# Kernel tuning notes

Measured on AMD Instinct MI355X. Metric: run time of the kernel, lower is better.

## Reference

```python
import jax, jax.numpy as jnp
import numpy as np

VOC_SIZE = 32768
DIM = 512
NUM_TOPK = 64
BATCH = 4096


def setup_inputs() -> dict:
    key = jax.random.key(0)
    ks = jax.random.split(key, 8)
    lim = 1.0 / np.sqrt(DIM)  # kaiming_uniform(a=sqrt(5)) on [V, d] -> U(-1/sqrt(d), 1/sqrt(d))
    x = jax.random.normal(ks[0], (BATCH, DIM), dtype=jnp.float32)
    codebook = jax.random.uniform(ks[1], (VOC_SIZE, DIM), dtype=jnp.float32, minval=-lim, maxval=lim)
    Wq = jax.random.uniform(ks[2], (DIM, DIM), dtype=jnp.float32, minval=-lim, maxval=lim)
    bq = jax.random.uniform(ks[3], (DIM,), dtype=jnp.float32, minval=-lim, maxval=lim)
    Wk = jax.random.uniform(ks[4], (DIM, DIM), dtype=jnp.float32, minval=-lim, maxval=lim)
    bk = jax.random.uniform(ks[5], (DIM,), dtype=jnp.float32, minval=-lim, maxval=lim)
    Wv = jax.random.uniform(ks[6], (DIM, DIM), dtype=jnp.float32, minval=-lim, maxval=lim)
    bv = jax.random.uniform(ks[7], (DIM,), dtype=jnp.float32, minval=-lim, maxval=lim)
    return {"x": x, "codebook": codebook, "Wq": Wq, "bq": bq,
            "Wk": Wk, "bk": bk, "Wv": Wv, "bv": bv}


def reference(x, codebook, Wq, bq, Wk, bk, Wv, bv):
    # projections (torch Linear with weight stored pre-transposed as [in, out])
    q = x @ Wq + bq              # [B, d]
    k = codebook @ Wk + bk       # [V, d]
    v = codebook @ Wv + bv       # [V, d]

    dots = jnp.einsum('bd,kd->bk', q, k)              # [B, V]
    top, _ = jax.lax.top_k(dots, NUM_TOPK)            # [B, num_topk]
    thresh = top[..., -1:]                            # k-th largest value per row
    mask_value = -jnp.finfo(dots.dtype).max
    dots = jnp.where(dots < thresh, mask_value, dots)
    attn = jax.nn.softmax(dots, axis=-1)              # [B, V]
    out = jnp.einsum('bk,kd->bd', attn, v)            # [B, d]
    return out
```

## Files before the change

### kernel.cpp

```cpp
#include <hip/hip_runtime.h>
#include <cstdint>

#define VOC   32768
#define DIM   512
#define TOPK  64
#define BATCH 4096

#define KSIG     2.45f
#define EPS_SEL  0.012f
#define CAND_CAP 512
#define RES_CAP  256
#define FCAP     1024

typedef unsigned short u16;
typedef __attribute__((ext_vector_type(8))) short bf16x8;
typedef __attribute__((ext_vector_type(4))) float f32x4;

__device__ __forceinline__ u16 f2bf(float f) {
    unsigned u = __float_as_uint(f);
    unsigned r = (u + 0x7FFFu + ((u >> 16) & 1u)) >> 16;
    return (u16)r;
}
__device__ __forceinline__ float bf2f(u16 h) {
    return __uint_as_float(((unsigned)h) << 16);
}
__device__ __forceinline__ unsigned enc16(u16 h) {
    return (h & 0x8000u) ? (unsigned)((u16)~h) : (unsigned)(h | 0x8000u);
}
__device__ __forceinline__ float dec16(unsigned s16) {
    u16 h = (s16 & 0x8000u) ? (u16)(s16 ^ 0x8000u) : (u16)(~s16);
    return bf2f(h);
}

__device__ __forceinline__ void async16(const void* g, void* l) {
    __builtin_amdgcn_global_load_lds(
        (const __attribute__((address_space(1))) void*)g,
        (__attribute__((address_space(3))) void*)l, 16, 0, 0);
}

template <bool BT, bool F64ACC>
__global__ __launch_bounds__(256)
void gemm64(const float* __restrict__ A, const float* __restrict__ B,
            const float* __restrict__ bias, float* __restrict__ C,
            int M, int N, int K)
{
    const int KS = 16;
    __shared__ float As[KS][68];
    __shared__ float Bs[KS][64];

    const int tid = threadIdx.x;
    const int m0 = blockIdx.y * 64;
    const int n0 = blockIdx.x * 64;
    const int ty = tid >> 4;
    const int tx = tid & 15;

    float acc[4][4];
    double acc64[4][4];
#pragma unroll
    for (int i = 0; i < 4; i++)
#pragma unroll
        for (int j = 0; j < 4; j++) { acc[i][j] = 0.f; if (F64ACC) acc64[i][j] = 0.0; }

    for (int kt = 0; kt < K; kt += KS) {
        {
            int row = tid >> 2, kq = tid & 3;
            const float4 av = *(const float4*)(A + (size_t)(m0 + row) * K + kt + kq * 4);
            As[kq * 4 + 0][row] = av.x;
            As[kq * 4 + 1][row] = av.y;
            As[kq * 4 + 2][row] = av.z;
            As[kq * 4 + 3][row] = av.w;
        }
        if (!BT) {
            int krow = tid >> 4, nq = tid & 15;
            *(float4*)&Bs[krow][nq * 4] =
                *(const float4*)(B + (size_t)(kt + krow) * N + n0 + nq * 4);
        } else {
            int nrow = tid >> 2, kq = tid & 3;
            const float4 bv = *(const float4*)(B + (size_t)(n0 + nrow) * K + kt + kq * 4);
            Bs[kq * 4 + 0][nrow] = bv.x;
            Bs[kq * 4 + 1][nrow] = bv.y;
            Bs[kq * 4 + 2][nrow] = bv.z;
            Bs[kq * 4 + 3][nrow] = bv.w;
        }
        __syncthreads();

#pragma unroll
        for (int kk = 0; kk < KS; kk++) {
            float4 a = *(const float4*)&As[kk][ty * 4];
            float4 b = *(const float4*)&Bs[kk][tx * 4];
            float av[4] = {a.x, a.y, a.z, a.w};
            float bv[4] = {b.x, b.y, b.z, b.w};
#pragma unroll
            for (int i = 0; i < 4; i++)
#pragma unroll
                for (int j = 0; j < 4; j++)
                    acc[i][j] += av[i] * bv[j];
        }
        __syncthreads();
        if (F64ACC) {
#pragma unroll
            for (int i = 0; i < 4; i++)
#pragma unroll
                for (int j = 0; j < 4; j++) { acc64[i][j] += (double)acc[i][j]; acc[i][j] = 0.f; }
        }
    }

    float4 bb = make_float4(0.f, 0.f, 0.f, 0.f);
    if (bias) bb = *(const float4*)(bias + n0 + tx * 4);
#pragma unroll
    for (int i = 0; i < 4; i++) {
        float4 o;
        o.x = (F64ACC ? (float)acc64[i][0] : acc[i][0]) + bb.x;
        o.y = (F64ACC ? (float)acc64[i][1] : acc[i][1]) + bb.y;
        o.z = (F64ACC ? (float)acc64[i][2] : acc[i][2]) + bb.z;
        o.w = (F64ACC ? (float)acc64[i][3] : acc[i][3]) + bb.w;
        *(float4*)(C + (size_t)(m0 + ty * 4 + i) * N + n0 + tx * 4) = o;
    }
}

__global__ void zero_ws(unsigned* __restrict__ p, int n)
{
    int i = blockIdx.x * 256 + threadIdx.x;
    if (i < n) p[i] = 0u;
}

__device__ __forceinline__ void pack_rows_dev(int bid, int tid,
        const float* __restrict__ src, u16* __restrict__ hi,
        u16* __restrict__ lo, int R, int log2R)
{
    int idx = bid * 256 + tid;
    int c8  = idx >> log2R;
    int row = idx & (R - 1);
    const float* sp = src + (size_t)row * DIM + c8 * 8;
    float xv[8];
    *(float4*)&xv[0] = *(const float4*)sp;
    *(float4*)&xv[4] = *(const float4*)(sp + 4);
    int ks = c8 >> 2, ch = c8 & 3;
    size_t ob = ((size_t)(ks * 4 + ch) * R + row) * 8;
    u16 h[8], l[8];
#pragma unroll
    for (int j = 0; j < 8; j++) {
        h[j] = f2bf(xv[j]);
        l[j] = f2bf(xv[j] - bf2f(h[j]));
    }
    *(uint4*)(hi + ob) = *(const uint4*)h;
    if (lo) *(uint4*)(lo + ob) = *(const uint4*)l;
}

__device__ __forceinline__ void pack_bT_dev(int bid, int tid,
        const float* __restrict__ W, u16* __restrict__ hi, u16* __restrict__ lo)
{
    int idx = bid * 256 + tid;
    int n  = idx & (DIM - 1);
    int c8 = idx >> 9;
    int ks = c8 >> 2, ch = c8 & 3;
    size_t ob = ((size_t)(ks * 4 + ch) * DIM + n) * 8;
    u16 h[8], l[8];
#pragma unroll
    for (int j = 0; j < 8; j++) {
        float x = W[(size_t)(c8 * 8 + j) * DIM + n];
        h[j] = f2bf(x);
        l[j] = f2bf(x - bf2f(h[j]));
    }
    *(uint4*)(hi + ob) = *(const uint4*)h;
    *(uint4*)(lo + ob) = *(const uint4*)l;
}

__device__ __forceinline__ void cbar_dev(int bid, int tid,
        const float* __restrict__ cb, float* __restrict__ cbarsum)
{
    const int r0 = bid * 128;
    float s0 = 0.f, s1 = 0.f;
    for (int r = 0; r < 128; r++) {
        const float* rp = cb + (size_t)(r0 + r) * DIM;
        s0 += rp[tid];
        s1 += rp[tid + 256];
    }
    atomicAdd(&cbarsum[tid], s0);
    atomicAdd(&cbarsum[tid + 256], s1);
}

__device__ __forceinline__ void bias_fold_dev(int bid, int tid,
        const float* __restrict__ bq, const float* __restrict__ Wk,
        float* __restrict__ bqk)
{
    const int lane = tid & 63, wave = tid >> 6;
    const int j = bid * 4 + wave;
    const float* wr = Wk + (size_t)j * DIM + lane * 8;
    const float* bp = bq + lane * 8;
    double s = 0.0;
#pragma unroll
    for (int t = 0; t < 8; t++) s += (double)bp[t] * (double)wr[t];
#pragma unroll
    for (int off = 32; off > 0; off >>= 1) s += __shfl_down(s, off);
    if (lane == 0) bqk[j] = (float)s;
}

__device__ __forceinline__ void rowstats_dev(int bid, int tid,
        const float* __restrict__ q2, const float* __restrict__ cbarsum,
        float* __restrict__ trow, float* __restrict__ sigrow)
{
    const int lane = tid & 63, wave = tid >> 6;
    const int row = bid * 4 + wave;
    const float* qp = q2 + (size_t)row * DIM + lane * 8;
    float4 a0 = *(const float4*)qp, a1 = *(const float4*)(qp + 4);
    const float* cp = cbarsum + lane * 8;
    float4 c0 = *(const float4*)cp, c1 = *(const float4*)(cp + 4);
    float mu = a0.x*c0.x + a0.y*c0.y + a0.z*c0.z + a0.w*c0.w
             + a1.x*c1.x + a1.y*c1.y + a1.z*c1.z + a1.w*c1.w;
    float nr = a0.x*a0.x + a0.y*a0.y + a0.z*a0.z + a0.w*a0.w
             + a1.x*a1.x + a1.y*a1.y + a1.z*a1.z + a1.w*a1.w;
#pragma unroll
    for (int off = 32; off > 0; off >>= 1) {
        mu += __shfl_down(mu, off);
        nr += __shfl_down(nr, off);
    }
    if (lane == 0) {
        mu *= (1.f / VOC);
        float sig = sqrtf(nr * (1.f / 1536.f));
        trow[row] = mu + KSIG * sig;
        sigrow[row] = sig;
    }
}

__global__ __launch_bounds__(256)
void fused_prep(const float* __restrict__ x, const float* __restrict__ Wqk,
                const float* __restrict__ codebook, const float* __restrict__ Wv,
                const float* __restrict__ bq, const float* __restrict__ Wk,
                u16* __restrict__ xh, u16* __restrict__ xl,
                u16* __restrict__ wqkh, u16* __restrict__ wqkl,
                u16* __restrict__ cbh, u16* __restrict__ wvh,
                u16* __restrict__ wvl, float* __restrict__ cbarsum,
                float* __restrict__ bqk)
{
    const int b = blockIdx.x, tid = threadIdx.x;
    if (b < 1024)       pack_rows_dev(b, tid, x, xh, xl, BATCH, 12);
    else if (b < 1152)  pack_bT_dev(b - 1024, tid, Wqk, wqkh, wqkl);
    else if (b < 9344)  pack_rows_dev(b - 1152, tid, codebook, cbh, nullptr, VOC, 15);
    else if (b < 9472)  pack_bT_dev(b - 9344, tid, Wv, wvh, wvl);
    else if (b < 9728)  cbar_dev(b - 9472, tid, codebook, cbarsum);
    else                bias_fold_dev(b - 9728, tid, bq, Wk, bqk);
}

__global__ __launch_bounds__(256)
void fused_q2post(const float* __restrict__ q2, const float* __restrict__ cbarsum,
                  float* __restrict__ trow, float* __restrict__ sigrow,
                  u16* __restrict__ q2h)
{
    const int b = blockIdx.x, tid = threadIdx.x;
    if (b < 1024) rowstats_dev(b, tid, q2, cbarsum, trow, sigrow);
    else          pack_rows_dev(b - 1024, tid, q2, q2h, nullptr, BATCH, 12);
}

__global__ __launch_bounds__(256, 4)
void mfma_dots(const u16* __restrict__ Ah, const u16* __restrict__ Bh,
               const float* __restrict__ trow, unsigned* __restrict__ candBuf,
               unsigned* __restrict__ counters)
{
    __shared__ u16 lds[2 * 8192];

    const int tid  = threadIdx.x;
    const int lane = tid & 63;
    const int wave = tid >> 6;
    const int wm = wave >> 1, wn = wave & 1;
    const int lr = lane & 15;
    const int q  = lane >> 4;

    const int L   = blockIdx.x;
    const int xcd = L & 7;
    const int j   = L >> 3;
    const int m0  = (xcd * 4 + (j & 3)) * 128;
    const int n0  = (j >> 2) * 128;

    const int a  = wave >> 1;
    const u16* src = a ? Bh : Ah;
    const int rb   = a ? n0 : m0;
    const size_t R = a ? (size_t)VOC : (size_t)BATCH;
    const int i0   = (wave & 1) * 4;

    const size_t gstep = (size_t)4 * R * 8;
    const u16* gp0 = src + ((size_t)(((i0 + 0) >> 1)) * R + rb + ((i0 + 0) & 1) * 64 + lane) * 8;
    const u16* gp1 = src + ((size_t)(((i0 + 1) >> 1)) * R + rb + ((i0 + 1) & 1) * 64 + lane) * 8;
    const u16* gp2 = src + ((size_t)(((i0 + 2) >> 1)) * R + rb + ((i0 + 2) & 1) * 64 + lane) * 8;
    const u16* gp3 = src + ((size_t)(((i0 + 3) >> 1)) * R + rb + ((i0 + 3) & 1) * 64 + lane) * 8;
    const int loff0 = a * 4096 + (i0 + 0) * 512 + lane * 8;
    const int loff1 = a * 4096 + (i0 + 1) * 512 + lane * 8;
    const int loff2 = a * 4096 + (i0 + 2) * 512 + lane * 8;
    const int loff3 = a * 4096 + (i0 + 3) * 512 + lane * 8;

#define ISSUE(b)                                                              \
    {                                                                         \
        async16(gp0, &lds[(b) * 8192 + loff0]); gp0 += gstep;                 \
        async16(gp1, &lds[(b) * 8192 + loff1]); gp1 += gstep;                 \
        async16(gp2, &lds[(b) * 8192 + loff2]); gp2 += gstep;                 \
        async16(gp3, &lds[(b) * 8192 + loff3]); gp3 += gstep;                 \
    }

    f32x4 acc[4][4] = {};

    ISSUE(0)
    ISSUE(1)

    for (int s = 0; s < 16; s++) {
        if (s < 15) __builtin_amdgcn_s_waitcnt(0x0F74);
        else        __builtin_amdgcn_s_waitcnt(0x0F70);
        __builtin_amdgcn_s_barrier();
        const u16* base = &lds[(s & 1) * 8192];

        bf16x8 ah[4];
#pragma unroll
        for (int mt = 0; mt < 4; mt++)
            ah[mt] = *(const bf16x8*)&base[q * 1024 + (wm * 64 + mt * 16 + lr) * 8];

        __builtin_amdgcn_s_setprio(1);
#pragma unroll
        for (int nt = 0; nt < 3; nt++) {
            bf16x8 bh = *(const bf16x8*)&base[4096 + q * 1024 + (wn * 64 + nt * 16 + lr) * 8];
#pragma unroll
            for (int mt = 0; mt < 4; mt++)
                acc[mt][nt] = __builtin_amdgcn_mfma_f32_16x16x32_bf16(ah[mt], bh, acc[mt][nt], 0, 0, 0);
        }
        bf16x8 bh3 = *(const bf16x8*)&base[4096 + q * 1024 + (wn * 64 + 3 * 16 + lr) * 8];
        __builtin_amdgcn_s_setprio(0);

        __builtin_amdgcn_s_waitcnt(0xC07F);
        __builtin_amdgcn_s_barrier();
        __builtin_amdgcn_sched_barrier(0);
        if (s < 14) ISSUE(s & 1)

        __builtin_amdgcn_s_setprio(1);
#pragma unroll
        for (int mt = 0; mt < 4; mt++)
            acc[mt][3] = __builtin_amdgcn_mfma_f32_16x16x32_bf16(ah[mt], bh3, acc[mt][3], 0, 0, 0);
        __builtin_amdgcn_s_setprio(0);
    }
#undef ISSUE

#pragma unroll
    for (int mt = 0; mt < 4; mt++) {
#pragma unroll
        for (int r = 0; r < 4; r++) {
            int rowg = m0 + wm * 64 + mt * 16 + q * 4 + r;
            float tr = trow[rowg];
#pragma unroll
            for (int nt = 0; nt < 4; nt++) {
                float val = acc[mt][nt][r];
                if (val >= tr) {
                    unsigned slot = atomicAdd(&counters[rowg], 1u);
                    if (slot < CAND_CAP) {
                        unsigned s16 = enc16(f2bf(val));
                        candBuf[(size_t)rowg * CAND_CAP + slot] =
                            (s16 << 16) | (unsigned)(n0 + wn * 64 + nt * 16 + lr);
                    }
                }
            }
        }
    }
}

__global__ __launch_bounds__(256, 3)
void mfma_out(const u16* __restrict__ Ah, const u16* __restrict__ Al,
              const u16* __restrict__ Bh, const u16* __restrict__ Bl,
              const float* __restrict__ bias, float* __restrict__ Cout, int Ma)
{
    __shared__ u16 lds[2 * 12288];

    const int tid  = threadIdx.x;
    const int lane = tid & 63;
    const int wave = tid >> 6;
    const int wm = wave >> 1, wn = wave & 1;
    const int m0 = blockIdx.y * 128, n0 = blockIdx.x * 64;
    const int lr = lane & 15;
    const int q  = lane >> 4;
    const size_t R = (size_t)Ma;

    f32x4 acc[4][2] = {};

#define VISSUE(ks, b)                                                          \
    {                                                                          \
        _Pragma("unroll")                                                      \
        for (int i_ = 0; i_ < 2; i_++) {                                       \
            int u_ = tid + i_ * 256;                                           \
            size_t ai_ = ((size_t)((ks) * 4 + (u_ >> 7)) * R + m0 + (u_ & 127)) * 8; \
            async16(Ah + ai_, &lds[(b) * 12288 + u_ * 8]);                     \
            async16(Al + ai_, &lds[(b) * 12288 + 6144 + u_ * 8]);              \
        }                                                                      \
        {                                                                      \
            int u_ = tid;                                                      \
            size_t bi_ = ((size_t)((ks) * 4 + (u_ >> 6)) * DIM + n0 + (u_ & 63)) * 8; \
            async16(Bh + bi_, &lds[(b) * 12288 + 4096 + u_ * 8]);              \
            async16(Bl + bi_, &lds[(b) * 12288 + 10240 + u_ * 8]);             \
        }                                                                      \
    }

    VISSUE(0, 0)

    for (int ks = 0; ks < 16; ks++) {
        __syncthreads();
        if (ks < 15) VISSUE(ks + 1, (ks + 1) & 1)
        const u16* base = &lds[(ks & 1) * 12288];

        bf16x8 ah[4], al[4];
#pragma unroll
        for (int mt = 0; mt < 4; mt++) {
            int row = wm * 64 + mt * 16 + lr;
            ah[mt] = *(const bf16x8*)&base[q * 1024 + row * 8];
            al[mt] = *(const bf16x8*)&base[6144 + q * 1024 + row * 8];
        }
#pragma unroll
        for (int nt = 0; nt < 2; nt++) {
            int col = wn * 32 + nt * 16 + lr;
            bf16x8 bh = *(const bf16x8*)&base[4096 + q * 512 + col * 8];
            bf16x8 bl = *(const bf16x8*)&base[10240 + q * 512 + col * 8];
#pragma unroll
            for (int mt = 0; mt < 4; mt++) {
                acc[mt][nt] = __builtin_amdgcn_mfma_f32_16x16x32_bf16(ah[mt], bh, acc[mt][nt], 0, 0, 0);
                acc[mt][nt] = __builtin_amdgcn_mfma_f32_16x16x32_bf16(ah[mt], bl, acc[mt][nt], 0, 0, 0);
                acc[mt][nt] = __builtin_amdgcn_mfma_f32_16x16x32_bf16(al[mt], bh, acc[mt][nt], 0, 0, 0);
            }
        }
    }
#undef VISSUE

#pragma unroll
    for (int mt = 0; mt < 4; mt++)
#pragma unroll
        for (int nt = 0; nt < 2; nt++) {
            int col = n0 + wn * 32 + nt * 16 + lr;
            float bb = bias[col];
#pragma unroll
            for (int r = 0; r < 4; r++) {
                int rowg = m0 + wm * 64 + mt * 16 + q * 4 + r;
                Cout[(size_t)rowg * DIM + col] = acc[mt][nt][r] + bb;
            }
        }
}

__global__ __launch_bounds__(256)
void select8(const unsigned* __restrict__ candBuf, const unsigned* __restrict__ counters,
             const float* __restrict__ trow, const float* __restrict__ sigrow,
             const float* __restrict__ q2, const float* __restrict__ codebook,
             float* __restrict__ y, u16* __restrict__ yh, u16* __restrict__ yl)
{
    __shared__ unsigned recs[CAND_CAP];
    __shared__ unsigned list[RES_CAP];
    __shared__ unsigned hist[256];
    __shared__ unsigned long long keys[FCAP];
    __shared__ float q2s[DIM];
    __shared__ float wArr[FCAP];
    __shared__ float yrow[DIM];
    __shared__ float redf[256];
    __shared__ unsigned redu[256];
    __shared__ unsigned s_R, s_b1, s_rem, s_thr, s_cnt;

    const int tid  = threadIdx.x;
    const int lane = tid & 63;
    const int wave = tid >> 6;
    const int row  = blockIdx.x;

    for (int i = tid; i < DIM; i += 256) q2s[i] = q2[(size_t)row * DIM + i];

    const unsigned cnt = counters[row];
    bool fb = (cnt < TOPK || cnt > CAND_CAP);
    int selCount = 0;
    float invZ = 1.f;

    if (!fb) {
        for (int i = tid; i < CAND_CAP; i += 256)
            recs[i] = (i < (int)cnt) ? candBuf[(size_t)row * CAND_CAP + i] : 0u;
        if (tid == 0) s_R = 0;
        hist[tid] = 0;
        __syncthreads();

#pragma unroll
        for (int e = 0; e < 2; e++) {
            int i = tid + e * 256;
            if (i < (int)cnt) atomicAdd(&hist[recs[i] >> 24], 1u);
        }
        __syncthreads();
        if (tid == 0) {
            unsigned c = 0; int b = 255;
            for (; b > 0; b--) {
                unsigned h = hist[b];
                if (c + h >= TOPK) break;
                c += h;
            }
            s_b1 = (unsigned)b; s_rem = TOPK - c;
        }
        __syncthreads();
        const unsigned b1 = s_b1, rem = s_rem;
        hist[tid] = 0;
        __syncthreads();

#pragma unroll
        for (int e = 0; e < 2; e++) {
            int i = tid + e * 256;
            if (i < (int)cnt && (recs[i] >> 24) == b1)
                atomicAdd(&hist[(recs[i] >> 16) & 0xFFu], 1u);
        }
        __syncthreads();
        if (tid == 0) {
            unsigned c = 0; int b = 255;
            for (; b > 0; b--) {
                unsigned h = hist[b];
                if (c + h >= rem) break;
                c += h;
            }
            s_thr = (b1 << 8) | (unsigned)b;
        }
        __syncthreads();

        const float a64  = dec16(s_thr);
        const float band = a64 - 2.f * EPS_SEL;
        if (trow[row] > band) fb = true;

        if (!fb) {
#pragma unroll
            for (int e = 0; e < 2; e++) {
                int i = tid + e * 256;
                if (i < (int)cnt && dec16(recs[i] >> 16) >= band) {
                    unsigned p = atomicAdd(&s_R, 1u);
                    if (p < RES_CAP) list[p] = recs[i];
                }
            }
            __syncthreads();
            const int R = (int)s_R;
            if (R > RES_CAP) fb = true;

            if (!fb) {
                for (int c = wave; c < R; c += 4) {
                    unsigned idx = list[c] & 0xFFFFu;
                    const float* cb = codebook + (size_t)idx * DIM + lane * 8;
                    float4 c0 = *(const float4*)cb, c1 = *(const float4*)(cb + 4);
                    const float* qp = &q2s[lane * 8];
                    float4 a0 = *(const float4*)qp, a1 = *(const float4*)(qp + 4);
                    double s = (double)a0.x * c0.x + (double)a0.y * c0.y
                             + (double)a0.z * c0.z + (double)a0.w * c0.w
                             + (double)a1.x * c1.x + (double)a1.y * c1.y
                             + (double)a1.z * c1.z + (double)a1.w * c1.w;
#pragma unroll
                    for (int off = 32; off > 0; off >>= 1) s += __shfl_down(s, off);
                    if (lane == 0) {
                        float val = (float)s;
                        unsigned b = __float_as_uint(val);
                        unsigned sk = (b & 0x80000000u) ? ~b : (b | 0x80000000u);
                        keys[c] = ((unsigned long long)(~sk) << 32) | idx;
                    }
                }
                if (tid >= R && tid < RES_CAP) keys[tid] = ~0ULL;
                __syncthreads();

                for (int k = 2; k <= RES_CAP; k <<= 1) {
                    for (int j = k >> 1; j > 0; j >>= 1) {
                        int ixj = tid ^ j;
                        if (ixj > tid) {
                            unsigned long long a = keys[tid], b2 = keys[ixj];
                            if (((tid & k) == 0) ? (a > b2) : (a < b2)) { keys[tid] = b2; keys[ixj] = a; }
                        }
                        __syncthreads();
                    }
                }

                const unsigned threshInv = (unsigned)(keys[TOPK - 1] >> 32);
                unsigned sk0 = ~(unsigned)(keys[0] >> 32);
                const float vmax = __uint_as_float((sk0 & 0x80000000u) ? (sk0 & 0x7FFFFFFFu) : ~sk0);

                unsigned hi = (unsigned)(keys[tid] >> 32);
                bool sel = (hi <= threshInv);
                unsigned sk = ~hi;
                float val = __uint_as_float((sk & 0x80000000u) ? (sk & 0x7FFFFFFFu) : ~sk);
                float w = sel ? expf(val - vmax) : 0.f;
                wArr[tid] = w;
                redf[tid] = w;
                redu[tid] = sel ? 1u : 0u;
                __syncthreads();
                for (int s = 128; s > 0; s >>= 1) {
                    if (tid < s) { redf[tid] += redf[tid + s]; redu[tid] += redu[tid + s]; }
                    __syncthreads();
                }
                invZ = 1.0f / redf[0];
                selCount = (int)redu[0];
            }
        }
    }

    if (fb) {
        const float sig = sigrow[row];
        float tf = trow[row] - 0.35f * sig;
        unsigned fcnt = 0;

        for (int it = 0; it < 16; it++) {
            if (tid == 0) s_cnt = 0;
            __syncthreads();
            for (int i = tid; i < VOC; i += 256) {
                const float* cb = codebook + (size_t)i * DIM;
                double s = 0.0;
                for (int d = 0; d < DIM; d += 4) {
                    float4 c4 = *(const float4*)(cb + d);
                    s += (double)q2s[d + 0] * (double)c4.x + (double)q2s[d + 1] * (double)c4.y
                       + (double)q2s[d + 2] * (double)c4.z + (double)q2s[d + 3] * (double)c4.w;
                }
                float vv = (float)s;
                if (vv >= tf) {
                    unsigned p = atomicAdd(&s_cnt, 1u);
                    if (p < FCAP) {
                        unsigned b = __float_as_uint(vv);
                        unsigned sk = (b & 0x80000000u) ? ~b : (b | 0x80000000u);
                        keys[p] = ((unsigned long long)(~sk) << 32) | (unsigned)i;
                    }
                }
            }
            __syncthreads();
            fcnt = s_cnt;
            if (fcnt > FCAP) { tf += 0.15f * sig; continue; }
            if (fcnt < TOPK) { tf -= 0.35f * sig; continue; }
            break;
        }
        if (fcnt > FCAP) fcnt = FCAP;
        for (int i = tid; i < FCAP; i += 256)
            if (i >= (int)fcnt) keys[i] = ~0ULL;
        __syncthreads();

        for (int k = 2; k <= FCAP; k <<= 1) {
            for (int j = k >> 1; j > 0; j >>= 1) {
#pragma unroll
                for (int e = 0; e < 4; e++) {
                    int i = tid + e * 256;
                    int ixj = i ^ j;
                    if (ixj > i) {
                        unsigned long long a = keys[i], b = keys[ixj];
                        if (((i & k) == 0) ? (a > b) : (a < b)) { keys[i] = b; keys[ixj] = a; }
                    }
                }
                __syncthreads();
            }
        }

        const unsigned threshInv = (unsigned)(keys[TOPK - 1] >> 32);
        unsigned sk0 = ~(unsigned)(keys[0] >> 32);
        const float vmax = __uint_as_float((sk0 & 0x80000000u) ? (sk0 & 0x7FFFFFFFu) : ~sk0);

        float lsum = 0.f; unsigned lcnt = 0;
        for (int i = tid; i < FCAP; i += 256) {
            unsigned hi = (unsigned)(keys[i] >> 32);
            bool sel = (hi <= threshInv);
            unsigned sk = ~hi;
            float vv = __uint_as_float((sk & 0x80000000u) ? (sk & 0x7FFFFFFFu) : ~sk);
            float w = sel ? expf(vv - vmax) : 0.f;
            wArr[i] = w;
            lsum += w; lcnt += sel ? 1u : 0u;
        }
        redf[tid] = lsum; redu[tid] = lcnt;
        __syncthreads();
        for (int s = 128; s > 0; s >>= 1) {
            if (tid < s) { redf[tid] += redf[tid + s]; redu[tid] += redu[tid + s]; }
            __syncthreads();
        }
        invZ = 1.f / redf[0];
        selCount = (int)redu[0];
    }

    for (int d = tid; d < DIM; d += 256) {
        float acc = 0.f;
        for (int i = 0; i < selCount; i++) {
            unsigned idx = (unsigned)(keys[i] & 0xFFFFFFFFu);
            acc += wArr[i] * codebook[(size_t)idx * DIM + d];
        }
        float v = acc * invZ;
        y[(size_t)row * DIM + d] = v;
        yrow[d] = v;
    }
    __syncthreads();
    if (tid < 64) {
        const int c8 = tid;
        u16 h[8], l[8];
#pragma unroll
        for (int j = 0; j < 8; j++) {
            float xv = yrow[c8 * 8 + j];
            h[j] = f2bf(xv);
            l[j] = f2bf(xv - bf2f(h[j]));
        }
        size_t ob = ((size_t)c8 * BATCH + row) * 8;
        *(uint4*)(yh + ob) = *(const uint4*)h;
        *(uint4*)(yl + ob) = *(const uint4*)l;
    }
}

extern "C" void kernel_launch(void* const* d_in, const int* in_sizes, int n_in,
                              void* d_out, int out_size, void* d_ws, size_t ws_size,
                              hipStream_t stream)
{
    const float* x        = (const float*)d_in[0];
    const float* codebook = (const float*)d_in[1];
    const float* Wq       = (const float*)d_in[2];
    const float* bq       = (const float*)d_in[3];
    const float* Wk       = (const float*)d_in[4];
    const float* Wv       = (const float*)d_in[6];
    const float* bv       = (const float*)d_in[7];
    float* out = (float*)d_out;

    float* q2   = (float*)d_ws;
    float* Wqk  = q2   + (size_t)BATCH * DIM;
    float* bqk  = Wqk  + (size_t)DIM * DIM;
    float* y    = bqk  + 1024;
    float* trow = y    + (size_t)BATCH * DIM;
    float* sigr = trow + BATCH;
    unsigned* counters = (unsigned*)(sigr + BATCH);
    unsigned* flags    = counters + BATCH;
    float* cbarsum     = (float*)(flags + BATCH);
    unsigned* candBuf  = (unsigned*)(cbarsum + 512);
    u16* q2h = (u16*)(candBuf + (size_t)BATCH * CAND_CAP);
    u16* cbh = q2h + (size_t)BATCH * DIM;
    u16* yh  = cbh + (size_t)VOC * DIM;
    u16* yl  = yh  + (size_t)BATCH * DIM;
    u16* wvh = yl  + (size_t)BATCH * DIM;
    u16* wvl = wvh + (size_t)DIM * DIM;

    u16* xh   = yh;
    u16* xl   = yl;
    u16* wqkh = (u16*)candBuf;
    u16* wqkl = wqkh + (size_t)DIM * DIM;

    dim3 blk(256);

    zero_ws<<<dim3(34), blk, 0, stream>>>(counters, BATCH * 2 + 512);

    gemm64<true, true><<<dim3(DIM / 64, DIM / 64), blk, 0, stream>>>(
        Wq, Wk, nullptr, Wqk, DIM, DIM, DIM);

    fused_prep<<<dim3(9856), blk, 0, stream>>>(
        x, Wqk, codebook, Wv, bq, Wk,
        xh, xl, wqkh, wqkl, cbh, wvh, wvl, cbarsum, bqk);

    mfma_out<<<dim3(DIM / 64, BATCH / 128), blk, 0, stream>>>(
        xh, xl, wqkh, wqkl, bqk, q2, BATCH);

    fused_q2post<<<dim3(2048), blk, 0, stream>>>(q2, cbarsum, trow, sigr, q2h);

    mfma_dots<<<dim3(8192), blk, 0, stream>>>(q2h, cbh, trow, candBuf, counters);

    select8<<<dim3(BATCH), blk, 0, stream>>>(
        candBuf, counters, trow, sigr, q2, codebook, y, yh, yl);

    mfma_out<<<dim3(DIM / 64, BATCH / 128), blk, 0, stream>>>(
        yh, yl, wvh, wvl, bv, out, BATCH);
}
```

Baseline: 663.3 us.

## Split row selection into lean fast-path kernel and separate flagged fallback kernel

The per-row select kernel is split in two. The fast candidate path keeps only RES_CAP-sized key and weight buffers and writes a flag for rows that need it. A second kernel runs the full-vocabulary fallback scan only for flagged rows. This shrinks LDS and register use in the common kernel so more blocks can be resident, and it drops the unused fp32 y write. The cost is an extra launch of BATCH blocks that mostly exit at once, and the flags buffer must be zeroed beforehand.

```diff
diff --git a/kernel.cpp b/kernel.cpp
--- a/kernel.cpp
+++ b/kernel.cpp
@@ -36,6 +36,24 @@
     __builtin_amdgcn_global_load_lds(
         (const __attribute__((address_space(1))) void*)g,
         (__attribute__((address_space(3))) void*)l, 16, 0, 0);
+}
+
+__device__ __forceinline__ void pack_y_tail(int tid, int row,
+        const float* __restrict__ yrow, u16* __restrict__ yh, u16* __restrict__ yl)
+{
+    if (tid < 64) {
+        const int c8 = tid;
+        u16 h[8], l[8];
+#pragma unroll
+        for (int j = 0; j < 8; j++) {
+            float xv = yrow[c8 * 8 + j];
+            h[j] = f2bf(xv);
+            l[j] = f2bf(xv - bf2f(h[j]));
+        }
+        size_t ob = ((size_t)c8 * BATCH + row) * 8;
+        *(uint4*)(yh + ob) = *(const uint4*)h;
+        *(uint4*)(yl + ob) = *(const uint4*)l;
+    }
 }
 
 template <bool BT, bool F64ACC>
@@ -437,228 +455,152 @@
 }
 
 __global__ __launch_bounds__(256)
-void select8(const unsigned* __restrict__ candBuf, const unsigned* __restrict__ counters,
-             const float* __restrict__ trow, const float* __restrict__ sigrow,
-             const float* __restrict__ q2, const float* __restrict__ codebook,
-             float* __restrict__ y, u16* __restrict__ yh, u16* __restrict__ yl)
+void select6(const unsigned* __restrict__ candBuf, const unsigned* __restrict__ counters,
+             const float* __restrict__ trow, const float* __restrict__ q2,
+             const float* __restrict__ codebook, unsigned* __restrict__ flags,
+             u16* __restrict__ yh, u16* __restrict__ yl)
 {
     __shared__ unsigned recs[CAND_CAP];
     __shared__ unsigned list[RES_CAP];
     __shared__ unsigned hist[256];
-    __shared__ unsigned long long keys[FCAP];
+    __shared__ unsigned long long keys[RES_CAP];
     __shared__ float q2s[DIM];
-    __shared__ float wArr[FCAP];
+    __shared__ float wArr[RES_CAP];
     __shared__ float yrow[DIM];
     __shared__ float redf[256];
     __shared__ unsigned redu[256];
-    __shared__ unsigned s_R, s_b1, s_rem, s_thr, s_cnt;
+    __shared__ unsigned s_R;
+    __shared__ unsigned s_b1, s_rem, s_thr;
 
     const int tid  = threadIdx.x;
     const int lane = tid & 63;
     const int wave = tid >> 6;
     const int row  = blockIdx.x;
 
+    const unsigned cnt = counters[row];
+    if (cnt < TOPK || cnt > CAND_CAP) {
+        if (tid == 0) flags[row] = 1u;
+        return;
+    }
     for (int i = tid; i < DIM; i += 256) q2s[i] = q2[(size_t)row * DIM + i];
-
-    const unsigned cnt = counters[row];
-    bool fb = (cnt < TOPK || cnt > CAND_CAP);
-    int selCount = 0;
-    float invZ = 1.f;
-
-    if (!fb) {
-        for (int i = tid; i < CAND_CAP; i += 256)
-            recs[i] = (i < (int)cnt) ? candBuf[(size_t)row * CAND_CAP + i] : 0u;
-        if (tid == 0) s_R = 0;
-        hist[tid] = 0;
-        __syncthreads();
-
-#pragma unroll
-        for (int e = 0; e < 2; e++) {
-            int i = tid + e * 256;
-            if (i < (int)cnt) atomicAdd(&hist[recs[i] >> 24], 1u);
-        }
-        __syncthreads();
-        if (tid == 0) {
-            unsigned c = 0; int b = 255;
-            for (; b > 0; b--) {
-                unsigned h = hist[b];
-                if (c + h >= TOPK) break;
-                c += h;
-            }
-            s_b1 = (unsigned)b; s_rem = TOPK - c;
-        }
-        __syncthreads();
-        const unsigned b1 = s_b1, rem = s_rem;
-        hist[tid] = 0;
-        __syncthreads();
-
-#pragma unroll
-        for (int e = 0; e < 2; e++) {
-            int i = tid + e * 256;
-            if (i < (int)cnt && (recs[i] >> 24) == b1)
-                atomicAdd(&hist[(recs[i] >> 16) & 0xFFu], 1u);
-        }
-        __syncthreads();
-        if (tid == 0) {
-            unsigned c = 0; int b = 255;
-            for (; b > 0; b--) {
-                unsigned h = hist[b];
-                if (c + h >= rem) break;
-                c += h;
-            }
-            s_thr = (b1 << 8) | (unsigned)b;
-        }
-        __syncthreads();
-
-        const float a64  = dec16(s_thr);
-        const float band = a64 - 2.f * EPS_SEL;
-        if (trow[row] > band) fb = true;
-
-        if (!fb) {
-#pragma unroll
-            for (int e = 0; e < 2; e++) {
-                int i = tid + e * 256;
-                if (i < (int)cnt && dec16(recs[i] >> 16) >= band) {
-                    unsigned p = atomicAdd(&s_R, 1u);
-                    if (p < RES_CAP) list[p] = recs[i];
-                }
+    for (int i = tid; i < CAND_CAP; i += 256)
+        recs[i] = (i < (int)cnt) ? candBuf[(size_t)row * CAND_CAP + i] : 0u;
+    if (tid == 0) s_R = 0;
+    hist[tid] = 0;
+    __syncthreads();
+
+#pragma unroll
+    for (int e = 0; e < 2; e++) {
+        int i = tid + e * 256;
+        if (i < (int)cnt) atomicAdd(&hist[recs[i] >> 24], 1u);
+    }
+    __syncthreads();
+    if (tid == 0) {
+        unsigned c = 0; int b = 255;
+        for (; b > 0; b--) {
+            unsigned h = hist[b];
+            if (c + h >= TOPK) break;
+            c += h;
+        }
+        s_b1 = (unsigned)b; s_rem = TOPK - c;
+    }
+    __syncthreads();
+    const unsigned b1 = s_b1, rem = s_rem;
+    hist[tid] = 0;
+    __syncthreads();
+
+#pragma unroll
+    for (int e = 0; e < 2; e++) {
+        int i = tid + e * 256;
+        if (i < (int)cnt && (recs[i] >> 24) == b1)
+            atomicAdd(&hist[(recs[i] >> 16) & 0xFFu], 1u);
+    }
+    __syncthreads();
+    if (tid == 0) {
+        unsigned c = 0; int b = 255;
+        for (; b > 0; b--) {
+            unsigned h = hist[b];
+            if (c + h >= rem) break;
+            c += h;
+        }
+        s_thr = (b1 << 8) | (unsigned)b;
+    }
+    __syncthreads();
+
+    const float a64  = dec16(s_thr);
+    const float band = a64 - 2.f * EPS_SEL;
+    if (trow[row] > band) {
+        if (tid == 0) flags[row] = 1u;
+        return;
+    }
+
+#pragma unroll
+    for (int e = 0; e < 2; e++) {
+        int i = tid + e * 256;
+        if (i < (int)cnt && dec16(recs[i] >> 16) >= band) {
+            unsigned p = atomicAdd(&s_R, 1u);
+            if (p < RES_CAP) list[p] = recs[i];
+        }
+    }
+    __syncthreads();
+    const int R = (int)s_R;
+    if (R > RES_CAP) {
+        if (tid == 0) flags[row] = 1u;
+        return;
+    }
+
+    for (int c = wave; c < R; c += 4) {
+        unsigned idx = list[c] & 0xFFFFu;
+        const float* cb = codebook + (size_t)idx * DIM + lane * 8;
+        float4 c0 = *(const float4*)cb, c1 = *(const float4*)(cb + 4);
+        const float* qp = &q2s[lane * 8];
+        float4 a0 = *(const float4*)qp, a1 = *(const float4*)(qp + 4);
+        double s = (double)a0.x * c0.x + (double)a0.y * c0.y
+                 + (double)a0.z * c0.z + (double)a0.w * c0.w
+                 + (double)a1.x * c1.x + (double)a1.y * c1.y
+                 + (double)a1.z * c1.z + (double)a1.w * c1.w;
+#pragma unroll
+        for (int off = 32; off > 0; off >>= 1) s += __shfl_down(s, off);
+        if (lane == 0) {
+            float val = (float)s;
+            unsigned b = __float_as_uint(val);
+            unsigned sk = (b & 0x80000000u) ? ~b : (b | 0x80000000u);
+            keys[c] = ((unsigned long long)(~sk) << 32) | idx;
+        }
+    }
+    if (tid >= R && tid < RES_CAP) keys[tid] = ~0ULL;
+    __syncthreads();
+
+    for (int k = 2; k <= RES_CAP; k <<= 1) {
+        for (int j = k >> 1; j > 0; j >>= 1) {
+            int ixj = tid ^ j;
+            if (ixj > tid) {
+                unsigned long long a = keys[tid], b2 = keys[ixj];
+                if (((tid & k) == 0) ? (a > b2) : (a < b2)) { keys[tid] = b2; keys[ixj] = a; }
             }
             __syncthreads();
-            const int R = (int)s_R;
-            if (R > RES_CAP) fb = true;
-
-            if (!fb) {
-                for (int c = wave; c < R; c += 4) {
-                    unsigned idx = list[c] & 0xFFFFu;
-                    const float* cb = codebook + (size_t)idx * DIM + lane * 8;
-                    float4 c0 = *(const float4*)cb, c1 = *(const float4*)(cb + 4);
-                    const float* qp = &q2s[lane * 8];
-                    float4 a0 = *(const float4*)qp, a1 = *(const float4*)(qp + 4);
-                    double s = (double)a0.x * c0.x + (double)a0.y * c0.y
-                             + (double)a0.z * c0.z + (double)a0.w * c0.w
-                             + (double)a1.x * c1.x + (double)a1.y * c1.y
-                             + (double)a1.z * c1.z + (double)a1.w * c1.w;
-#pragma unroll
-                    for (int off = 32; off > 0; off >>= 1) s += __shfl_down(s, off);
-                    if (lane == 0) {
-                        float val = (float)s;
-                        unsigned b = __float_as_uint(val);
-                        unsigned sk = (b & 0x80000000u) ? ~b : (b | 0x80000000u);
-                        keys[c] = ((unsigned long long)(~sk) << 32) | idx;
-                    }
-                }
-                if (tid >= R && tid < RES_CAP) keys[tid] = ~0ULL;
-                __syncthreads();
-
-                for (int k = 2; k <= RES_CAP; k <<= 1) {
-                    for (int j = k >> 1; j > 0; j >>= 1) {
-                        int ixj = tid ^ j;
-                        if (ixj > tid) {
-                            unsigned long long a = keys[tid], b2 = keys[ixj];
-                            if (((tid & k) == 0) ? (a > b2) : (a < b2)) { keys[tid] = b2; keys[ixj] = a; }
-                        }
-                        __syncthreads();
-                    }
-                }
-
-                const unsigned threshInv = (unsigned)(keys[TOPK - 1] >> 32);
-                unsigned sk0 = ~(unsigned)(keys[0] >> 32);
-                const float vmax = __uint_as_float((sk0 & 0x80000000u) ? (sk0 & 0x7FFFFFFFu) : ~sk0);
-
-                unsigned hi = (unsigned)(keys[tid] >> 32);
-                bool sel = (hi <= threshInv);
-                unsigned sk = ~hi;
-                float val = __uint_as_float((sk & 0x80000000u) ? (sk & 0x7FFFFFFFu) : ~sk);
-                float w = sel ? expf(val - vmax) : 0.f;
-                wArr[tid] = w;
-                redf[tid] = w;
-                redu[tid] = sel ? 1u : 0u;
-                __syncthreads();
-                for (int s = 128; s > 0; s >>= 1) {
-                    if (tid < s) { redf[tid] += redf[tid + s]; redu[tid] += redu[tid + s]; }
-                    __syncthreads();
-                }
-                invZ = 1.0f / redf[0];
-                selCount = (int)redu[0];
-            }
-        }
-    }
-
-    if (fb) {
-        const float sig = sigrow[row];
-        float tf = trow[row] - 0.35f * sig;
-        unsigned fcnt = 0;
-
-        for (int it = 0; it < 16; it++) {
-            if (tid == 0) s_cnt = 0;
-            __syncthreads();
-            for (int i = tid; i < VOC; i += 256) {
-                const float* cb = codebook + (size_t)i * DIM;
-                double s = 0.0;
-                for (int d = 0; d < DIM; d += 4) {
-                    float4 c4 = *(const float4*)(cb + d);
-                    s += (double)q2s[d + 0] * (double)c4.x + (double)q2s[d + 1] * (double)c4.y
-                       + (double)q2s[d + 2] * (double)c4.z + (double)q2s[d + 3] * (double)c4.w;
-                }
-                float vv = (float)s;
-                if (vv >= tf) {
-                    unsigned p = atomicAdd(&s_cnt, 1u);
-                    if (p < FCAP) {
-                        unsigned b = __float_as_uint(vv);
-                        unsigned sk = (b & 0x80000000u) ? ~b : (b | 0x80000000u);
-                        keys[p] = ((unsigned long long)(~sk) << 32) | (unsigned)i;
-                    }
-                }
-            }
-            __syncthreads();
-            fcnt = s_cnt;
-            if (fcnt > FCAP) { tf += 0.15f * sig; continue; }
-            if (fcnt < TOPK) { tf -= 0.35f * sig; continue; }
-            break;
-        }
-        if (fcnt > FCAP) fcnt = FCAP;
-        for (int i = tid; i < FCAP; i += 256)
-            if (i >= (int)fcnt) keys[i] = ~0ULL;
+        }
+    }
+
+    const unsigned threshInv = (unsigned)(keys[TOPK - 1] >> 32);
+    unsigned sk0 = ~(unsigned)(keys[0] >> 32);
+    const float vmax = __uint_as_float((sk0 & 0x80000000u) ? (sk0 & 0x7FFFFFFFu) : ~sk0);
+
+    unsigned hi = (unsigned)(keys[tid] >> 32);
+    bool sel = (hi <= threshInv);
+    unsigned sk = ~hi;
+    float val = __uint_as_float((sk & 0x80000000u) ? (sk & 0x7FFFFFFFu) : ~sk);
+    float w = sel ? expf(val - vmax) : 0.f;
+    wArr[tid] = w;
+    redf[tid] = w;
+    redu[tid] = sel ? 1u : 0u;
+    __syncthreads();
+    for (int s = 128; s > 0; s >>= 1) {
+        if (tid < s) { redf[tid] += redf[tid + s]; redu[tid] += redu[tid + s]; }
         __syncthreads();
-
-        for (int k = 2; k <= FCAP; k <<= 1) {
-            for (int j = k >> 1; j > 0; j >>= 1) {
-#pragma unroll
-                for (int e = 0; e < 4; e++) {
-                    int i = tid + e * 256;
-                    int ixj = i ^ j;
-                    if (ixj > i) {
-                        unsigned long long a = keys[i], b = keys[ixj];
-                        if (((i & k) == 0) ? (a > b) : (a < b)) { keys[i] = b; keys[ixj] = a; }
-                    }
-                }
-                __syncthreads();
-            }
-        }
-
-        const unsigned threshInv = (unsigned)(keys[TOPK - 1] >> 32);
-        unsigned sk0 = ~(unsigned)(keys[0] >> 32);
-        const float vmax = __uint_as_float((sk0 & 0x80000000u) ? (sk0 & 0x7FFFFFFFu) : ~sk0);
-
-        float lsum = 0.f; unsigned lcnt = 0;
-        for (int i = tid; i < FCAP; i += 256) {
-            unsigned hi = (unsigned)(keys[i] >> 32);
-            bool sel = (hi <= threshInv);
-            unsigned sk = ~hi;
-            float vv = __uint_as_float((sk & 0x80000000u) ? (sk & 0x7FFFFFFFu) : ~sk);
-            float w = sel ? expf(vv - vmax) : 0.f;
-            wArr[i] = w;
-            lsum += w; lcnt += sel ? 1u : 0u;
-        }
-        redf[tid] = lsum; redu[tid] = lcnt;
-        __syncthreads();
-        for (int s = 128; s > 0; s >>= 1) {
-            if (tid < s) { redf[tid] += redf[tid + s]; redu[tid] += redu[tid + s]; }
-            __syncthreads();
-        }
-        invZ = 1.f / redf[0];
-        selCount = (int)redu[0];
-    }
+    }
+    const float invZ = 1.0f / redf[0];
+    const int selCount = (int)redu[0];
 
     for (int d = tid; d < DIM; d += 256) {
         float acc = 0.f;
@@ -666,24 +608,115 @@
             unsigned idx = (unsigned)(keys[i] & 0xFFFFFFFFu);
             acc += wArr[i] * codebook[(size_t)idx * DIM + d];
         }
-        float v = acc * invZ;
-        y[(size_t)row * DIM + d] = v;
-        yrow[d] = v;
-    }
-    __syncthreads();
-    if (tid < 64) {
-        const int c8 = tid;
-        u16 h[8], l[8];
-#pragma unroll
-        for (int j = 0; j < 8; j++) {
-            float xv = yrow[c8 * 8 + j];
-            h[j] = f2bf(xv);
-            l[j] = f2bf(xv - bf2f(h[j]));
-        }
-        size_t ob = ((size_t)c8 * BATCH + row) * 8;
-        *(uint4*)(yh + ob) = *(const uint4*)h;
-        *(uint4*)(yl + ob) = *(const uint4*)l;
-    }
+        yrow[d] = acc * invZ;
+    }
+    __syncthreads();
+    pack_y_tail(tid, row, yrow, yh, yl);
+}
+
+__global__ __launch_bounds__(256)
+void fallback_row(const unsigned* __restrict__ flags, const float* __restrict__ q2,
+                  const float* __restrict__ codebook, const float* __restrict__ trow,
+                  const float* __restrict__ sigrow, u16* __restrict__ yh,
+                  u16* __restrict__ yl)
+{
+    const int row = blockIdx.x;
+    if (!flags[row]) return;
+
+    __shared__ float q2s[DIM];
+    __shared__ unsigned long long keys[FCAP];
+    __shared__ float wArr[FCAP];
+    __shared__ float yrow[DIM];
+    __shared__ float redf[256];
+    __shared__ unsigned redu[256];
+    __shared__ unsigned s_cnt;
+
+    const int tid = threadIdx.x;
+    for (int i = tid; i < DIM; i += 256) q2s[i] = q2[(size_t)row * DIM + i];
+    const float sig = sigrow[row];
+    float tf = trow[row] - 0.35f * sig;
+    unsigned cnt = 0;
+
+    for (int it = 0; it < 16; it++) {
+        if (tid == 0) s_cnt = 0;
+        __syncthreads();
+        for (int i = tid; i < VOC; i += 256) {
+            const float* cb = codebook + (size_t)i * DIM;
+            double s = 0.0;
+            for (int d = 0; d < DIM; d += 4) {
+                float4 c4 = *(const float4*)(cb + d);
+                s += (double)q2s[d + 0] * (double)c4.x + (double)q2s[d + 1] * (double)c4.y
+                   + (double)q2s[d + 2] * (double)c4.z + (double)q2s[d + 3] * (double)c4.w;
+            }
+            float vv = (float)s;
+            if (vv >= tf) {
+                unsigned p = atomicAdd(&s_cnt, 1u);
+                if (p < FCAP) {
+                    unsigned b = __float_as_uint(vv);
+                    unsigned sk = (b & 0x80000000u) ? ~b : (b | 0x80000000u);
+                    keys[p] = ((unsigned long long)(~sk) << 32) | (unsigned)i;
+                }
+            }
+        }
+        __syncthreads();
+        cnt = s_cnt;
+        if (cnt > FCAP) { tf += 0.15f * sig; continue; }
+        if (cnt < TOPK) { tf -= 0.35f * sig; continue; }
+        break;
+    }
+    if (cnt > FCAP) cnt = FCAP;
+    for (int i = tid; i < FCAP; i += 256)
+        if (i >= (int)cnt) keys[i] = ~0ULL;
+    __syncthreads();
+
+    for (int k = 2; k <= FCAP; k <<= 1) {
+        for (int j = k >> 1; j > 0; j >>= 1) {
+#pragma unroll
+            for (int e = 0; e < 4; e++) {
+                int i = tid + e * 256;
+                int ixj = i ^ j;
+                if (ixj > i) {
+                    unsigned long long a = keys[i], b = keys[ixj];
+                    if (((i & k) == 0) ? (a > b) : (a < b)) { keys[i] = b; keys[ixj] = a; }
+                }
+            }
+            __syncthreads();
+        }
+    }
+
+    const unsigned threshInv = (unsigned)(keys[TOPK - 1] >> 32);
+    unsigned sk0 = ~(unsigned)(keys[0] >> 32);
+    const float vmax = __uint_as_float((sk0 & 0x80000000u) ? (sk0 & 0x7FFFFFFFu) : ~sk0);
+
+    float lsum = 0.f; unsigned lcnt = 0;
+    for (int i = tid; i < FCAP; i += 256) {
+        unsigned hi = (unsigned)(keys[i] >> 32);
+        bool sel = (hi <= threshInv);
+        unsigned sk = ~hi;
+        float vv = __uint_as_float((sk & 0x80000000u) ? (sk & 0x7FFFFFFFu) : ~sk);
+        float w = sel ? expf(vv - vmax) : 0.f;
+        wArr[i] = w;
+        lsum += w; lcnt += sel ? 1u : 0u;
+    }
+    redf[tid] = lsum; redu[tid] = lcnt;
+    __syncthreads();
+    for (int s = 128; s > 0; s >>= 1) {
+        if (tid < s) { redf[tid] += redf[tid + s]; redu[tid] += redu[tid + s]; }
+        __syncthreads();
+    }
+    const float invZ = 1.f / redf[0];
+    const int selCount = (int)redu[0];
+
+    for (int d = tid; d < DIM; d += 256) {
+        float acc = 0.f;
+        for (int i = 0; i < selCount; i++) {
+            unsigned idx = (unsigned)(keys[i] & 0xFFFFFFFFu);
+            acc += wArr[i] * codebook[(size_t)idx * DIM + d];
+        }
+        yrow[d] = acc * invZ;
+    }
+    __syncthreads();
+    pack_y_tail(tid, row, yrow, yh, yl);
 }
 
 extern "C" void kernel_launch(void* const* d_in, const int* in_sizes, int n_in,
@@ -739,8 +772,10 @@
 
     mfma_dots<<<dim3(8192), blk, 0, stream>>>(q2h, cbh, trow, candBuf, counters);
 
-    select8<<<dim3(BATCH), blk, 0, stream>>>(
-        candBuf, counters, trow, sigr, q2, codebook, y, yh, yl);
+    select6<<<dim3(BATCH), blk, 0, stream>>>(
+        candBuf, counters, trow, q2, codebook, flags, yh, yl);
+    fallback_row<<<dim3(BATCH), blk, 0, stream>>>(
+        flags, q2, codebook, trow, sigr, yh, yl);
 
     mfma_out<<<dim3(DIM / 64, BATCH / 128), blk, 0, stream>>>(
         yh, yl, wvh, wvl, bv, out, BATCH);
```

New measurement: 653.9 us. About the same (-1.4%).
